# Performance work log

Hardware: AMD Instinct MI355X
Metric: run time of the kernel (lower is better)

Reference implementation:

```python
import jax, jax.numpy as jnp
import numpy as np

N_HEAD, QK_DIM, V_DIM = 8, 32, 32
INNER = N_HEAD * V_DIM  # 256
D_MODEL = 256
N_VAR = 2
NEG = -1e9
LN_EPS = 1e-5


def irregular_rope(q, t):
    # q: [BN, L, H, D], t: [BN, L]
    D = q.shape[-1]
    inv_freq = 1.0 / (10000.0 ** (jnp.arange(0, D, 2, dtype=jnp.float32) / D))  # [D/2]
    ang = t[:, :, None, None] * inv_freq[None, None, None, :]  # [BN, L, 1, D/2]
    cos, sin = jnp.cos(ang), jnp.sin(ang)
    q1, q2 = q[..., 0::2], q[..., 1::2]
    out = jnp.stack([q1 * cos - q2 * sin, q1 * sin + q2 * cos], axis=-1)
    return out.reshape(q.shape)


def layernorm(x, g, b):
    mu = jnp.mean(x, axis=-1, keepdims=True)
    var = jnp.mean((x - mu) ** 2, axis=-1, keepdims=True)
    return (x - mu) * jax.lax.rsqrt(var + LN_EPS) * g + b


def setup_inputs() -> dict:
    key = jax.random.key(0)
    ks = jax.random.split(key, 14)
    B, PN, PL = 16, 64, 128
    x = jax.random.normal(ks[0], (B, PN, PL, N_VAR), dtype=jnp.float32)
    t = jnp.sort(jax.random.uniform(ks[1], (B, PN, PL + 1), dtype=jnp.float32) * 100.0, axis=-1)
    mask = jax.random.randint(ks[2], (B, PN, PL + 1), 0, 2, dtype=jnp.int32)
    mask = mask.at[..., 0].set(1)  # emb token never masked
    s = 0.05
    return {
        "x": x, "t": t, "mask": mask,
        "emb_token": jnp.zeros((1, 1, 1, N_VAR), dtype=jnp.float32),
        "Wq": jax.random.normal(ks[3], (N_VAR, N_HEAD * QK_DIM), dtype=jnp.float32) * s,
        "Wk": jax.random.normal(ks[4], (N_VAR, N_HEAD * QK_DIM), dtype=jnp.float32) * s,
        "Wv": jax.random.normal(ks[5], (N_VAR, N_HEAD * V_DIM), dtype=jnp.float32) * s,
        "Wo": jax.random.normal(ks[6], (INNER, D_MODEL), dtype=jnp.float32) * s,
        "ln_g": jnp.ones((INNER,), dtype=jnp.float32),
        "ln_b": jnp.zeros((INNER,), dtype=jnp.float32),
        "W1": jax.random.normal(ks[7], (INNER, 4 * INNER), dtype=jnp.float32) * s,
        "b1": jnp.zeros((4 * INNER,), dtype=jnp.float32),
        "W2": jax.random.normal(ks[8], (4 * INNER, INNER), dtype=jnp.float32) * s,
        "b2": jnp.zeros((INNER,), dtype=jnp.float32),
    }


def reference(x, t, mask, emb_token, Wq, Wk, Wv, Wo, ln_g, ln_b, W1, b1, W2, b2):
    B, PN, PL, _ = x.shape
    L = PL + 1
    BN = B * PN
    emb = jnp.broadcast_to(emb_token, (B, PN, 1, N_VAR))
    _x = jnp.concatenate([emb, x], axis=2)  # [B, PN, L, 2]
    Q = (_x @ Wq).reshape(BN, L, N_HEAD, QK_DIM)
    K = (_x @ Wk).reshape(BN, L, N_HEAD, QK_DIM)
    V = (_x @ Wv).reshape(BN, L, N_HEAD, V_DIM)
    tt = t.reshape(BN, L)
    Q = irregular_rope(Q, tt)
    K = irregular_rope(K, tt)
    # attention: [BN, H, L, L]
    scores = jnp.einsum('blhd,bmhd->bhlm', Q, K) / jnp.sqrt(jnp.float32(QK_DIM))
    m = mask.reshape(BN, L).astype(jnp.float32)
    mask_mat = (m[:, :, None] * m[:, None, :])[:, None, :, :]  # [BN,1,L,L]
    scores = jnp.where(mask_mat > 0, scores, NEG)
    attn = jax.nn.softmax(scores, axis=-1)
    ctx = jnp.einsum('bhlm,bmhd->blhd', attn, V)  # [BN, L, H, Dv]
    last = ctx[:, 0].reshape(B, PN, INNER)  # emb-token output
    h = layernorm(last, ln_g, ln_b)
    h = jax.nn.relu(h @ W1 + b1) @ W2 + b2
    last = last + h
    return last @ Wo  # [B, PN, D_MODEL]
```

## Files before the change

### kernel.cpp

```cpp
#include <hip/hip_runtime.h>
#include <math.h>

#define LSEQ   129
#define PLEN   128
#define NHEAD  8
#define DHEAD  32
#define INNER  256
#define HID    1024

typedef _Float16 h2 __attribute__((ext_vector_type(2)));
typedef _Float16 h8 __attribute__((ext_vector_type(8)));

__device__ __forceinline__ float fdot2(h2 a, h2 b, float c) {
#if __has_builtin(__builtin_amdgcn_fdot2)
    return __builtin_amdgcn_fdot2(a, b, c, false);
#else
    return c + (float)a.x * (float)b.x + (float)a.y * (float)b.y;
#endif
}

__device__ __forceinline__ float dot8(h8 a, h8 b, float c) {
    h2 a0 = __builtin_shufflevector(a, a, 0, 1);
    h2 a1 = __builtin_shufflevector(a, a, 2, 3);
    h2 a2 = __builtin_shufflevector(a, a, 4, 5);
    h2 a3 = __builtin_shufflevector(a, a, 6, 7);
    h2 b0 = __builtin_shufflevector(b, b, 0, 1);
    h2 b1 = __builtin_shufflevector(b, b, 2, 3);
    h2 b2 = __builtin_shufflevector(b, b, 4, 5);
    h2 b3 = __builtin_shufflevector(b, b, 6, 7);
    c = fdot2(a0, b0, c);
    c = fdot2(a1, b1, c);
    c = fdot2(a2, b2, c);
    c = fdot2(a3, b3, c);
    return c;
}

__global__ __launch_bounds__(256) void attn_kernel(
    const float* __restrict__ x,
    const float* __restrict__ t,
    const int*   __restrict__ mask,
    const float* __restrict__ emb,
    const float* __restrict__ Wq,
    const float* __restrict__ Wk,
    const float* __restrict__ Wv,
    const float* __restrict__ W1,
    const float* __restrict__ W2,
    const float* __restrict__ Wo,
    float*       __restrict__ last,
    h8*          __restrict__ W1o,
    h8*          __restrict__ W2o,
    h8*          __restrict__ Woo)
{
    const int bn  = blockIdx.x;
    const int tid = threadIdx.x;

    {
        int g = bn * 256 + tid;
        if (g < 73728) {
            h8 v;
            if (g < 32768) {
                int c8 = g >> 10, j = g & 1023;
                const float* src = W1 + (8 * c8) * HID + j;
#pragma unroll
                for (int i = 0; i < 8; ++i) v[i] = (_Float16)src[i * HID];
                W1o[g] = v;
            } else if (g < 65536) {
                int l = g - 32768;
                int c8 = l >> 8, o = l & 255;
                const float* src = W2 + (8 * c8) * INNER + o;
#pragma unroll
                for (int i = 0; i < 8; ++i) v[i] = (_Float16)src[i * INNER];
                W2o[l] = v;
            } else {
                int l = g - 65536;
                int c8 = l >> 8, o = l & 255;
                const float* src = Wo + (8 * c8) * INNER + o;
#pragma unroll
                for (int i = 0; i < 8; ++i) v[i] = (_Float16)src[i * INNER];
                Woo[l] = v;
            }
        }
    }

    __shared__ float2 cs_s[16][132];
    __shared__ float2 x_s[132];
    __shared__ float4 ab_s[8][16];
    __shared__ float  sc_s[8][132];
    __shared__ int    mask_s[132];
    __shared__ float  hstat_s[8][3];

    const float* tb = t + bn * LSEQ;
    const float t0  = tb[0];
    const float e0 = emb[0], e1 = emb[1];

    if (tid < 130) {
        float2 v;
        if (tid == 0)        v = make_float2(e0, e1);
        else if (tid <= 128) v = ((const float2*)(x + bn * PLEN * 2))[tid - 1];
        else                 v = make_float2(0.f, 0.f);
        x_s[tid] = v;
    }
    if (tid < 129) mask_s[tid] = mask[bn * LSEQ + tid];

    for (int i = tid; i < 129 * 16; i += 256) {
        int m = i >> 4, j = i & 15;
        float invf = exp2f(-(float)j * 0.8304820237218407f);
        float sv, cv;
        __sincosf((tb[m] - t0) * invf, &sv, &cv);
        cs_s[j][m] = make_float2(cv, sv);
    }

    if (tid < 128) {
        int h = tid >> 4, j = tid & 15;
        int ce = h * 32 + 2 * j, co = ce + 1;
        float qe = e0 * Wq[ce] + e1 * Wq[256 + ce];
        float qo = e0 * Wq[co] + e1 * Wq[256 + co];
        float k0e = Wk[ce], k0o = Wk[co];
        float k1e = Wk[256 + ce], k1o = Wk[256 + co];
        const float sc = 0.17677669529663687f;
        ab_s[h][j] = make_float4((qe * k0e + qo * k0o) * sc,
                                 (qo * k0e - qe * k0o) * sc,
                                 (qe * k1e + qo * k1o) * sc,
                                 (qo * k1e - qe * k1o) * sc);
    }
    __syncthreads();

    const int lane = tid & 63;
    const int wv   = tid >> 6;
    const int h    = wv * 2 + (lane >> 5);
    const int l32  = lane & 31;

    float4 ab[16];
#pragma unroll
    for (int j = 0; j < 16; ++j) ab[j] = ab_s[h][j];

#pragma unroll
    for (int k = 0; k < 5; ++k) {
        int m = l32 + 32 * k;
        if (m < 129) {
            float2 xv = x_s[m];
            float accA = 0.f, accB = 0.f;
#pragma unroll
            for (int j = 0; j < 16; ++j) {
                float2 cs = cs_s[j][m];
                accA = fmaf(cs.x, ab[j].x, accA);
                accA = fmaf(cs.y, ab[j].y, accA);
                accB = fmaf(cs.x, ab[j].z, accB);
                accB = fmaf(cs.y, ab[j].w, accB);
            }
            sc_s[h][m] = accA * xv.x + accB * xv.y;
        }
    }
    __syncthreads();

    const int mask0 = mask_s[0];
    float se[5];
    float M = -1e30f;
#pragma unroll
    for (int k = 0; k < 5; ++k) {
        int m = l32 + 32 * k;
        float s;
        if (m < 129) {
            s = sc_s[h][m];
            if (mask0 == 0)          s = 0.f;
            else if (mask_s[m] == 0) s = -1e9f;
        } else s = -1e30f;
        se[k] = s;
        M = fmaxf(M, s);
    }
#pragma unroll
    for (int off = 16; off >= 1; off >>= 1) M = fmaxf(M, __shfl_xor(M, off, 64));

    float den = 0.f, S0 = 0.f, S1 = 0.f;
#pragma unroll
    for (int k = 0; k < 5; ++k) {
        int m = l32 + 32 * k;
        if (m < 129) {
            float e = __expf(se[k] - M);
            float2 xv = x_s[m];
            den += e;
            S0 = fmaf(e, xv.x, S0);
            S1 = fmaf(e, xv.y, S1);
        }
    }
#pragma unroll
    for (int off = 16; off >= 1; off >>= 1) {
        den += __shfl_xor(den, off, 64);
        S0  += __shfl_xor(S0,  off, 64);
        S1  += __shfl_xor(S1,  off, 64);
    }
    if (l32 == 0) {
        hstat_s[h][0] = den; hstat_s[h][1] = S0; hstat_s[h][2] = S1;
    }
    __syncthreads();

    {
        int hh = tid >> 5;
        float inv = 1.f / hstat_s[hh][0];
        last[bn * 256 + tid] =
            (hstat_s[hh][1] * Wv[tid] + hstat_s[hh][2] * Wv[256 + tid]) * inv;
    }
}

__global__ __launch_bounds__(1024) void mlp_kernel(
    const float* __restrict__ last,
    const float* __restrict__ ln_g,
    const float* __restrict__ ln_b,
    const h8*    __restrict__ W1o,
    const float* __restrict__ b1,
    const h8*    __restrict__ W2o,
    const float* __restrict__ b2,
    const h8*    __restrict__ Woo,
    float*       __restrict__ out)
{
    const int tid = threadIdx.x;
    const int r0  = blockIdx.x * 4;
    const int rg  = tid >> 8;
    const int ch  = tid & 255;

    __shared__ float x_s[4][INNER];
    __shared__ alignas(16) _Float16 h_h[4][INNER];
    __shared__ alignas(16) _Float16 y_h[4][HID];
    __shared__ alignas(16) _Float16 r_h[4][INNER];
    __shared__ float p_s[4][4][INNER];
    __shared__ float red_s[16][2];

    float xv = last[(r0 + rg) * INNER + ch];
    x_s[rg][ch] = xv;

    float s1 = xv, s2 = xv * xv;
#pragma unroll
    for (int off = 32; off >= 1; off >>= 1) {
        s1 += __shfl_xor(s1, off, 64);
        s2 += __shfl_xor(s2, off, 64);
    }
    const int wave = tid >> 6;
    if ((tid & 63) == 0) { red_s[wave][0] = s1; red_s[wave][1] = s2; }
    __syncthreads();

    {
        float t1 = red_s[4 * rg + 0][0] + red_s[4 * rg + 1][0] +
                   red_s[4 * rg + 2][0] + red_s[4 * rg + 3][0];
        float t2 = red_s[4 * rg + 0][1] + red_s[4 * rg + 1][1] +
                   red_s[4 * rg + 2][1] + red_s[4 * rg + 3][1];
        float mu  = t1 * (1.f / 256.f);
        float var = t2 * (1.f / 256.f) - mu * mu;
        float rs  = rsqrtf(var + 1e-5f);
        h_h[rg][ch] = (_Float16)((xv - mu) * rs * ln_g[ch] + ln_b[ch]);
    }
    __syncthreads();

    {
        float a0, a1v, a2v, a3;
        a0 = a1v = a2v = a3 = b1[tid];
        const h8* w = W1o + tid;
#pragma unroll 8
        for (int c8 = 0; c8 < 32; ++c8) {
            h8 wv = w[c8 * HID];
            h8 h0 = *(const h8*)&h_h[0][c8 * 8];
            h8 h1 = *(const h8*)&h_h[1][c8 * 8];
            h8 hh2 = *(const h8*)&h_h[2][c8 * 8];
            h8 h3 = *(const h8*)&h_h[3][c8 * 8];
            a0  = dot8(h0, wv, a0);
            a1v = dot8(h1, wv, a1v);
            a2v = dot8(hh2, wv, a2v);
            a3  = dot8(h3, wv, a3);
        }
        y_h[0][tid] = (_Float16)fmaxf(a0, 0.f);
        y_h[1][tid] = (_Float16)fmaxf(a1v, 0.f);
        y_h[2][tid] = (_Float16)fmaxf(a2v, 0.f);
        y_h[3][tid] = (_Float16)fmaxf(a3, 0.f);
    }
    __syncthreads();

    {
        float a0 = 0.f, a1v = 0.f, a2v = 0.f, a3 = 0.f;
        const h8* w = W2o + rg * 32 * INNER + ch;
#pragma unroll 8
        for (int i = 0; i < 32; ++i) {
            int c8 = rg * 32 + i;
            h8 wv = w[i * INNER];
            h8 y0 = *(const h8*)&y_h[0][c8 * 8];
            h8 y1 = *(const h8*)&y_h[1][c8 * 8];
            h8 y2 = *(const h8*)&y_h[2][c8 * 8];
            h8 y3 = *(const h8*)&y_h[3][c8 * 8];
            a0  = dot8(y0, wv, a0);
            a1v = dot8(y1, wv, a1v);
            a2v = dot8(y2, wv, a2v);
            a3  = dot8(y3, wv, a3);
        }
        p_s[rg][0][ch] = a0;
        p_s[rg][1][ch] = a1v;
        p_s[rg][2][ch] = a2v;
        p_s[rg][3][ch] = a3;
    }
    __syncthreads();

    {
        float rv = x_s[rg][ch] + b2[ch] +
                   p_s[0][rg][ch] + p_s[1][rg][ch] +
                   p_s[2][rg][ch] + p_s[3][rg][ch];
        r_h[rg][ch] = (_Float16)rv;
    }
    __syncthreads();

    {
        float a0 = 0.f, a1v = 0.f, a2v = 0.f, a3 = 0.f;
        const h8* w = Woo + rg * 8 * INNER + ch;
#pragma unroll
        for (int i = 0; i < 8; ++i) {
            int c8 = rg * 8 + i;
            h8 wv = w[i * INNER];
            h8 v0 = *(const h8*)&r_h[0][c8 * 8];
            h8 v1 = *(const h8*)&r_h[1][c8 * 8];
            h8 v2 = *(const h8*)&r_h[2][c8 * 8];
            h8 v3 = *(const h8*)&r_h[3][c8 * 8];
            a0  = dot8(v0, wv, a0);
            a1v = dot8(v1, wv, a1v);
            a2v = dot8(v2, wv, a2v);
            a3  = dot8(v3, wv, a3);
        }
        p_s[rg][0][ch] = a0;
        p_s[rg][1][ch] = a1v;
        p_s[rg][2][ch] = a2v;
        p_s[rg][3][ch] = a3;
    }
    __syncthreads();

    out[(r0 + rg) * INNER + ch] = p_s[0][rg][ch] + p_s[1][rg][ch] +
                                  p_s[2][rg][ch] + p_s[3][rg][ch];
}

extern "C" void kernel_launch(void* const* d_in, const int* in_sizes, int n_in,
                              void* d_out, int out_size, void* d_ws, size_t ws_size,
                              hipStream_t stream) {
    const float* x    = (const float*)d_in[0];
    const float* t    = (const float*)d_in[1];
    const int*   mask = (const int*)  d_in[2];
    const float* emb  = (const float*)d_in[3];
    const float* Wq   = (const float*)d_in[4];
    const float* Wk   = (const float*)d_in[5];
    const float* Wv   = (const float*)d_in[6];
    const float* Wo   = (const float*)d_in[7];
    const float* ln_g = (const float*)d_in[8];
    const float* ln_b = (const float*)d_in[9];
    const float* W1   = (const float*)d_in[10];
    const float* b1   = (const float*)d_in[11];
    const float* W2   = (const float*)d_in[12];
    const float* b2   = (const float*)d_in[13];
    float* out = (float*)d_out;

    const int BN = in_sizes[1] / LSEQ;

    char* ws = (char*)d_ws;
    float* last_ws = (float*)ws;
    h8* W1o = (h8*)(ws + (1u << 20));
    h8* W2o = (h8*)(ws + (1u << 20) + (512u << 10));
    h8* Woo = (h8*)(ws + (2u << 20));

    attn_kernel<<<BN, 256, 0, stream>>>(x, t, mask, emb, Wq, Wk, Wv,
                                        W1, W2, Wo, last_ws, W1o, W2o, Woo);
    mlp_kernel<<<BN / 4, 1024, 0, stream>>>(last_ws, ln_g, ln_b, W1o, b1,
                                            W2o, b2, Woo, out);
}
```

Baseline: 108.0 us.

## Fuse attention into MLP kernel and split weight repack into its own kernel

```diff
diff --git a/kernel.cpp b/kernel.cpp
--- a/kernel.cpp
+++ b/kernel.cpp
@@ -35,7 +35,52 @@
     return c;
 }
 
-__global__ __launch_bounds__(256) void attn_kernel(
+__global__ __launch_bounds__(256) void repack_kernel(
+    const float* __restrict__ W1, const float* __restrict__ W2,
+    const float* __restrict__ Wo,
+    h8* __restrict__ W1o, h8* __restrict__ W2o, h8* __restrict__ Woo)
+{
+    int g = blockIdx.x * 256 + threadIdx.x;
+    if (g >= 73728) return;
+    h8 v;
+    if (g < 32768) {
+        int c8 = g >> 10, j = g & 1023;
+        const float* src = W1 + (8 * c8) * HID + j;
+#pragma unroll
+        for (int i = 0; i < 8; ++i) v[i] = (_Float16)src[i * HID];
+        W1o[g] = v;
+    } else if (g < 65536) {
+        int l = g - 32768;
+        int c8 = l >> 8, o = l & 255;
+        const float* src = W2 + (8 * c8) * INNER + o;
+#pragma unroll
+        for (int i = 0; i < 8; ++i) v[i] = (_Float16)src[i * INNER];
+        W2o[l] = v;
+    } else {
+        int l = g - 65536;
+        int c8 = l >> 8, o = l & 255;
+        const float* src = Wo + (8 * c8) * INNER + o;
+#pragma unroll
+        for (int i = 0; i < 8; ++i) v[i] = (_Float16)src[i * INNER];
+        Woo[l] = v;
+    }
+}
+
+struct AttnSmem {
+    float2 cs[4][16][132];
+    float4 ab[4][8][16];
+    float2 xp[4][132];
+    float  sc[4][8][132];
+    int    mk[4][132];
+};
+struct MlpSmem {
+    _Float16 h[4][INNER];
+    _Float16 y[4][HID];
+    _Float16 r[4][INNER];
+    float    p[4][4][INNER];
+};
+
+__global__ __launch_bounds__(1024) void fused_kernel(
     const float* __restrict__ x,
     const float* __restrict__ t,
     const int*   __restrict__ mask,
@@ -43,167 +88,6 @@
     const float* __restrict__ Wq,
     const float* __restrict__ Wk,
     const float* __restrict__ Wv,
-    const float* __restrict__ W1,
-    const float* __restrict__ W2,
-    const float* __restrict__ Wo,
-    float*       __restrict__ last,
-    h8*          __restrict__ W1o,
-    h8*          __restrict__ W2o,
-    h8*          __restrict__ Woo)
-{
-    const int bn  = blockIdx.x;
-    const int tid = threadIdx.x;
-
-    {
-        int g = bn * 256 + tid;
-        if (g < 73728) {
-            h8 v;
-            if (g < 32768) {
-                int c8 = g >> 10, j = g & 1023;
-                const float* src = W1 + (8 * c8) * HID + j;
-#pragma unroll
-                for (int i = 0; i < 8; ++i) v[i] = (_Float16)src[i * HID];
-                W1o[g] = v;
-            } else if (g < 65536) {
-                int l = g - 32768;
-                int c8 = l >> 8, o = l & 255;
-                const float* src = W2 + (8 * c8) * INNER + o;
-#pragma unroll
-                for (int i = 0; i < 8; ++i) v[i] = (_Float16)src[i * INNER];
-                W2o[l] = v;
-            } else {
-                int l = g - 65536;
-                int c8 = l >> 8, o = l & 255;
-                const float* src = Wo + (8 * c8) * INNER + o;
-#pragma unroll
-                for (int i = 0; i < 8; ++i) v[i] = (_Float16)src[i * INNER];
-                Woo[l] = v;
-            }
-        }
-    }
-
-    __shared__ float2 cs_s[16][132];
-    __shared__ float2 x_s[132];
-    __shared__ float4 ab_s[8][16];
-    __shared__ float  sc_s[8][132];
-    __shared__ int    mask_s[132];
-    __shared__ float  hstat_s[8][3];
-
-    const float* tb = t + bn * LSEQ;
-    const float t0  = tb[0];
-    const float e0 = emb[0], e1 = emb[1];
-
-    if (tid < 130) {
-        float2 v;
-        if (tid == 0)        v = make_float2(e0, e1);
-        else if (tid <= 128) v = ((const float2*)(x + bn * PLEN * 2))[tid - 1];
-        else                 v = make_float2(0.f, 0.f);
-        x_s[tid] = v;
-    }
-    if (tid < 129) mask_s[tid] = mask[bn * LSEQ + tid];
-
-    for (int i = tid; i < 129 * 16; i += 256) {
-        int m = i >> 4, j = i & 15;
-        float invf = exp2f(-(float)j * 0.8304820237218407f);
-        float sv, cv;
-        __sincosf((tb[m] - t0) * invf, &sv, &cv);
-        cs_s[j][m] = make_float2(cv, sv);
-    }
-
-    if (tid < 128) {
-        int h = tid >> 4, j = tid & 15;
-        int ce = h * 32 + 2 * j, co = ce + 1;
-        float qe = e0 * Wq[ce] + e1 * Wq[256 + ce];
-        float qo = e0 * Wq[co] + e1 * Wq[256 + co];
-        float k0e = Wk[ce], k0o = Wk[co];
-        float k1e = Wk[256 + ce], k1o = Wk[256 + co];
-        const float sc = 0.17677669529663687f;
-        ab_s[h][j] = make_float4((qe * k0e + qo * k0o) * sc,
-                                 (qo * k0e - qe * k0o) * sc,
-                                 (qe * k1e + qo * k1o) * sc,
-                                 (qo * k1e - qe * k1o) * sc);
-    }
-    __syncthreads();
-
-    const int lane = tid & 63;
-    const int wv   = tid >> 6;
-    const int h    = wv * 2 + (lane >> 5);
-    const int l32  = lane & 31;
-
-    float4 ab[16];
-#pragma unroll
-    for (int j = 0; j < 16; ++j) ab[j] = ab_s[h][j];
-
-#pragma unroll
-    for (int k = 0; k < 5; ++k) {
-        int m = l32 + 32 * k;
-        if (m < 129) {
-            float2 xv = x_s[m];
-            float accA = 0.f, accB = 0.f;
-#pragma unroll
-            for (int j = 0; j < 16; ++j) {
-                float2 cs = cs_s[j][m];
-                accA = fmaf(cs.x, ab[j].x, accA);
-                accA = fmaf(cs.y, ab[j].y, accA);
-                accB = fmaf(cs.x, ab[j].z, accB);
-                accB = fmaf(cs.y, ab[j].w, accB);
-            }
-            sc_s[h][m] = accA * xv.x + accB * xv.y;
-        }
-    }
-    __syncthreads();
-
-    const int mask0 = mask_s[0];
-    float se[5];
-    float M = -1e30f;
-#pragma unroll
-    for (int k = 0; k < 5; ++k) {
-        int m = l32 + 32 * k;
-        float s;
-        if (m < 129) {
-            s = sc_s[h][m];
-            if (mask0 == 0)          s = 0.f;
-            else if (mask_s[m] == 0) s = -1e9f;
-        } else s = -1e30f;
-        se[k] = s;
-        M = fmaxf(M, s);
-    }
-#pragma unroll
-    for (int off = 16; off >= 1; off >>= 1) M = fmaxf(M, __shfl_xor(M, off, 64));
-
-    float den = 0.f, S0 = 0.f, S1 = 0.f;
-#pragma unroll
-    for (int k = 0; k < 5; ++k) {
-        int m = l32 + 32 * k;
-        if (m < 129) {
-            float e = __expf(se[k] - M);
-            float2 xv = x_s[m];
-            den += e;
-            S0 = fmaf(e, xv.x, S0);
-            S1 = fmaf(e, xv.y, S1);
-        }
-    }
-#pragma unroll
-    for (int off = 16; off >= 1; off >>= 1) {
-        den += __shfl_xor(den, off, 64);
-        S0  += __shfl_xor(S0,  off, 64);
-        S1  += __shfl_xor(S1,  off, 64);
-    }
-    if (l32 == 0) {
-        hstat_s[h][0] = den; hstat_s[h][1] = S0; hstat_s[h][2] = S1;
-    }
-    __syncthreads();
-
-    {
-        int hh = tid >> 5;
-        float inv = 1.f / hstat_s[hh][0];
-        last[bn * 256 + tid] =
-            (hstat_s[hh][1] * Wv[tid] + hstat_s[hh][2] * Wv[256 + tid]) * inv;
-    }
-}
-
-__global__ __launch_bounds__(1024) void mlp_kernel(
-    const float* __restrict__ last,
     const float* __restrict__ ln_g,
     const float* __restrict__ ln_b,
     const h8*    __restrict__ W1o,
@@ -218,26 +102,144 @@
     const int rg  = tid >> 8;
     const int ch  = tid & 255;
 
-    __shared__ float x_s[4][INNER];
-    __shared__ alignas(16) _Float16 h_h[4][INNER];
-    __shared__ alignas(16) _Float16 y_h[4][HID];
-    __shared__ alignas(16) _Float16 r_h[4][INNER];
-    __shared__ float p_s[4][4][INNER];
+    __shared__ alignas(16) char smem[sizeof(AttnSmem)];
+    __shared__ float hstat_s[4][8][3];
     __shared__ float red_s[16][2];
-
-    float xv = last[(r0 + rg) * INNER + ch];
-    x_s[rg][ch] = xv;
-
-    float s1 = xv, s2 = xv * xv;
-#pragma unroll
-    for (int off = 32; off >= 1; off >>= 1) {
-        s1 += __shfl_xor(s1, off, 64);
-        s2 += __shfl_xor(s2, off, 64);
-    }
-    const int wave = tid >> 6;
-    if ((tid & 63) == 0) { red_s[wave][0] = s1; red_s[wave][1] = s2; }
-    __syncthreads();
-
+    AttnSmem* A = reinterpret_cast<AttnSmem*>(smem);
+    MlpSmem*  M = reinterpret_cast<MlpSmem*>(smem);
+
+    const int bn = r0 + rg;
+    const float* tb = t + bn * LSEQ;
+    const float t0  = tb[0];
+    const float e0 = emb[0], e1 = emb[1];
+
+    if (ch < 130) {
+        float2 v;
+        if (ch == 0)        v = make_float2(e0, e1);
+        else if (ch <= 128) v = ((const float2*)(x + bn * PLEN * 2))[ch - 1];
+        else                v = make_float2(0.f, 0.f);
+        A->xp[rg][ch] = v;
+    }
+    if (ch < 129) A->mk[rg][ch] = mask[bn * LSEQ + ch];
+
+    for (int i = ch; i < 129 * 16; i += 256) {
+        int m = i >> 4, j = i & 15;
+        float invf = exp2f(-(float)j * 0.8304820237218407f);
+        float sv, cv;
+        __sincosf((tb[m] - t0) * invf, &sv, &cv);
+        A->cs[rg][j][m] = make_float2(cv, sv);
+    }
+
+    if (ch < 128) {
+        int h = ch >> 4, j = ch & 15;
+        int ce = h * 32 + 2 * j, co = ce + 1;
+        float qe = e0 * Wq[ce] + e1 * Wq[256 + ce];
+        float qo = e0 * Wq[co] + e1 * Wq[256 + co];
+        float k0e = Wk[ce], k0o = Wk[co];
+        float k1e = Wk[256 + ce], k1o = Wk[256 + co];
+        const float sc = 0.17677669529663687f;
+        A->ab[rg][h][j] = make_float4((qe * k0e + qo * k0o) * sc,
+                                      (qo * k0e - qe * k0o) * sc,
+                                      (qe * k1e + qo * k1o) * sc,
+                                      (qo * k1e - qe * k1o) * sc);
+    }
+    __syncthreads();
+
+    const int lane = tid & 63;
+    const int wg   = (tid >> 6) & 3;
+    const int h    = wg * 2 + (lane >> 5);
+    const int l32  = lane & 31;
+
+    {
+        float4 ab[16];
+#pragma unroll
+        for (int j = 0; j < 16; ++j) ab[j] = A->ab[rg][h][j];
+
+#pragma unroll
+        for (int k = 0; k < 5; ++k) {
+            int m = l32 + 32 * k;
+            if (m < 129) {
+                float2 xv2 = A->xp[rg][m];
+                float accA = 0.f, accB = 0.f;
+#pragma unroll
+                for (int j = 0; j < 16; ++j) {
+                    float2 cs = A->cs[rg][j][m];
+                    accA = fmaf(cs.x, ab[j].x, accA);
+                    accA = fmaf(cs.y, ab[j].y, accA);
+                    accB = fmaf(cs.x, ab[j].z, accB);
+                    accB = fmaf(cs.y, ab[j].w, accB);
+                }
+                A->sc[rg][h][m] = accA * xv2.x + accB * xv2.y;
+            }
+        }
+    }
+    __syncthreads();
+
+    {
+        const int mask0 = A->mk[rg][0];
+        float se[5];
+        float Mx = -1e30f;
+#pragma unroll
+        for (int k = 0; k < 5; ++k) {
+            int m = l32 + 32 * k;
+            float s;
+            if (m < 129) {
+                s = A->sc[rg][h][m];
+                if (mask0 == 0)            s = 0.f;
+                else if (A->mk[rg][m] == 0) s = -1e9f;
+            } else s = -1e30f;
+            se[k] = s;
+            Mx = fmaxf(Mx, s);
+        }
+#pragma unroll
+        for (int off = 16; off >= 1; off >>= 1)
+            Mx = fmaxf(Mx, __shfl_xor(Mx, off, 64));
+
+        float den = 0.f, S0 = 0.f, S1 = 0.f;
+#pragma unroll
+        for (int k = 0; k < 5; ++k) {
+            int m = l32 + 32 * k;
+            if (m < 129) {
+                float e = __expf(se[k] - Mx);
+                float2 xv2 = A->xp[rg][m];
+                den += e;
+                S0 = fmaf(e, xv2.x, S0);
+                S1 = fmaf(e, xv2.y, S1);
+            }
+        }
+#pragma unroll
+        for (int off = 16; off >= 1; off >>= 1) {
+            den += __shfl_xor(den, off, 64);
+            S0  += __shfl_xor(S0,  off, 64);
+            S1  += __shfl_xor(S1,  off, 64);
+        }
+        if (l32 == 0) {
+            hstat_s[rg][h][0] = den;
+            hstat_s[rg][h][1] = S0;
+            hstat_s[rg][h][2] = S1;
+        }
+    }
+    __syncthreads();
+
+    float xv;
+    {
+        int hh = ch >> 5;
+        float inv = 1.f / hstat_s[rg][hh][0];
+        xv = (hstat_s[rg][hh][1] * Wv[ch] +
+              hstat_s[rg][hh][2] * Wv[256 + ch]) * inv;
+    }
+
+    {
+        float s1 = xv, s2 = xv * xv;
+#pragma unroll
+        for (int off = 32; off >= 1; off >>= 1) {
+            s1 += __shfl_xor(s1, off, 64);
+            s2 += __shfl_xor(s2, off, 64);
+        }
+        const int wave = tid >> 6;
+        if ((tid & 63) == 0) { red_s[wave][0] = s1; red_s[wave][1] = s2; }
+    }
+    __syncthreads();
     {
         float t1 = red_s[4 * rg + 0][0] + red_s[4 * rg + 1][0] +
                    red_s[4 * rg + 2][0] + red_s[4 * rg + 3][0];
@@ -246,7 +248,7 @@
         float mu  = t1 * (1.f / 256.f);
         float var = t2 * (1.f / 256.f) - mu * mu;
         float rs  = rsqrtf(var + 1e-5f);
-        h_h[rg][ch] = (_Float16)((xv - mu) * rs * ln_g[ch] + ln_b[ch]);
+        M->h[rg][ch] = (_Float16)((xv - mu) * rs * ln_g[ch] + ln_b[ch]);
     }
     __syncthreads();
 
@@ -257,19 +259,19 @@
 #pragma unroll 8
         for (int c8 = 0; c8 < 32; ++c8) {
             h8 wv = w[c8 * HID];
-            h8 h0 = *(const h8*)&h_h[0][c8 * 8];
-            h8 h1 = *(const h8*)&h_h[1][c8 * 8];
-            h8 hh2 = *(const h8*)&h_h[2][c8 * 8];
-            h8 h3 = *(const h8*)&h_h[3][c8 * 8];
+            h8 h0 = *(const h8*)&M->h[0][c8 * 8];
+            h8 h1 = *(const h8*)&M->h[1][c8 * 8];
+            h8 hh2 = *(const h8*)&M->h[2][c8 * 8];
+            h8 h3 = *(const h8*)&M->h[3][c8 * 8];
             a0  = dot8(h0, wv, a0);
             a1v = dot8(h1, wv, a1v);
             a2v = dot8(hh2, wv, a2v);
             a3  = dot8(h3, wv, a3);
         }
-        y_h[0][tid] = (_Float16)fmaxf(a0, 0.f);
-        y_h[1][tid] = (_Float16)fmaxf(a1v, 0.f);
-        y_h[2][tid] = (_Float16)fmaxf(a2v, 0.f);
-        y_h[3][tid] = (_Float16)fmaxf(a3, 0.f);
+        M->y[0][tid] = (_Float16)fmaxf(a0, 0.f);
+        M->y[1][tid] = (_Float16)fmaxf(a1v, 0.f);
+        M->y[2][tid] = (_Float16)fmaxf(a2v, 0.f);
+        M->y[3][tid] = (_Float16)fmaxf(a3, 0.f);
     }
     __syncthreads();
 
@@ -280,27 +282,27 @@
         for (int i = 0; i < 32; ++i) {
             int c8 = rg * 32 + i;
             h8 wv = w[i * INNER];
-            h8 y0 = *(const h8*)&y_h[0][c8 * 8];
-            h8 y1 = *(const h8*)&y_h[1][c8 * 8];
-            h8 y2 = *(const h8*)&y_h[2][c8 * 8];
-            h8 y3 = *(const h8*)&y_h[3][c8 * 8];
+            h8 y0 = *(const h8*)&M->y[0][c8 * 8];
+            h8 y1 = *(const h8*)&M->y[1][c8 * 8];
+            h8 y2 = *(const h8*)&M->y[2][c8 * 8];
+            h8 y3 = *(const h8*)&M->y[3][c8 * 8];
             a0  = dot8(y0, wv, a0);
             a1v = dot8(y1, wv, a1v);
             a2v = dot8(y2, wv, a2v);
             a3  = dot8(y3, wv, a3);
         }
-        p_s[rg][0][ch] = a0;
-        p_s[rg][1][ch] = a1v;
-        p_s[rg][2][ch] = a2v;
-        p_s[rg][3][ch] = a3;
-    }
-    __syncthreads();
-
-    {
-        float rv = x_s[rg][ch] + b2[ch] +
-                   p_s[0][rg][ch] + p_s[1][rg][ch] +
-                   p_s[2][rg][ch] + p_s[3][rg][ch];
-        r_h[rg][ch] = (_Float16)rv;
+        M->p[rg][0][ch] = a0;
+        M->p[rg][1][ch] = a1v;
+        M->p[rg][2][ch] = a2v;
+        M->p[rg][3][ch] = a3;
+    }
+    __syncthreads();
+
+    {
+        float rv = xv + b2[ch] +
+                   M->p[0][rg][ch] + M->p[1][rg][ch] +
+                   M->p[2][rg][ch] + M->p[3][rg][ch];
+        M->r[rg][ch] = (_Float16)rv;
     }
     __syncthreads();
 
@@ -311,24 +313,24 @@
         for (int i = 0; i < 8; ++i) {
             int c8 = rg * 8 + i;
             h8 wv = w[i * INNER];
-            h8 v0 = *(const h8*)&r_h[0][c8 * 8];
-            h8 v1 = *(const h8*)&r_h[1][c8 * 8];
-            h8 v2 = *(const h8*)&r_h[2][c8 * 8];
-            h8 v3 = *(const h8*)&r_h[3][c8 * 8];
+            h8 v0 = *(const h8*)&M->r[0][c8 * 8];
+            h8 v1 = *(const h8*)&M->r[1][c8 * 8];
+            h8 v2 = *(const h8*)&M->r[2][c8 * 8];
+            h8 v3 = *(const h8*)&M->r[3][c8 * 8];
             a0  = dot8(v0, wv, a0);
             a1v = dot8(v1, wv, a1v);
             a2v = dot8(v2, wv, a2v);
             a3  = dot8(v3, wv, a3);
         }
-        p_s[rg][0][ch] = a0;
-        p_s[rg][1][ch] = a1v;
-        p_s[rg][2][ch] = a2v;
-        p_s[rg][3][ch] = a3;
-    }
-    __syncthreads();
-
-    out[(r0 + rg) * INNER + ch] = p_s[0][rg][ch] + p_s[1][rg][ch] +
-                                  p_s[2][rg][ch] + p_s[3][rg][ch];
+        M->p[rg][0][ch] = a0;
+        M->p[rg][1][ch] = a1v;
+        M->p[rg][2][ch] = a2v;
+        M->p[rg][3][ch] = a3;
+    }
+    __syncthreads();
+
+    out[(r0 + rg) * INNER + ch] = M->p[0][rg][ch] + M->p[1][rg][ch] +
+                                  M->p[2][rg][ch] + M->p[3][rg][ch];
 }
 
 extern "C" void kernel_launch(void* const* d_in, const int* in_sizes, int n_in,
@@ -353,13 +355,12 @@
     const int BN = in_sizes[1] / LSEQ;
 
     char* ws = (char*)d_ws;
-    float* last_ws = (float*)ws;
-    h8* W1o = (h8*)(ws + (1u << 20));
-    h8* W2o = (h8*)(ws + (1u << 20) + (512u << 10));
-    h8* Woo = (h8*)(ws + (2u << 20));
-
-    attn_kernel<<<BN, 256, 0, stream>>>(x, t, mask, emb, Wq, Wk, Wv,
-                                        W1, W2, Wo, last_ws, W1o, W2o, Woo);
-    mlp_kernel<<<BN / 4, 1024, 0, stream>>>(last_ws, ln_g, ln_b, W1o, b1,
-                                            W2o, b2, Woo, out);
-}
+    h8* W1o = (h8*)ws;
+    h8* W2o = (h8*)(ws + (512u << 10));
+    h8* Woo = (h8*)(ws + (1u << 20));
+
+    repack_kernel<<<288, 256, 0, stream>>>(W1, W2, Wo, W1o, W2o, Woo);
+    fused_kernel<<<BN / 4, 1024, 0, stream>>>(x, t, mask, emb, Wq, Wk, Wv,
+                                              ln_g, ln_b, W1o, b1, W2o, b2,
+                                              Woo, out);
+}
```

Result: slower. 111.9 us (+3.6%).
